# Optimization experiments

Hardware: AMD Instinct MI355X
Metric: run time of the kernel (lower is better)

## Reference

```python
import jax, jax.numpy as jnp
import numpy as np

D_MODEL = 2048
N_HEADS = 16
N_KV = 4
D_HEAD = 128
D1 = 64
D2 = 64
WSIZE = 1024
EPS = 1e-6
ROPE_BASE = 10000.0


def _rmsnorm(x):
    # RMSNorm over last dim, no affine weight
    return x * jax.lax.rsqrt(jnp.mean(x * x, axis=-1, keepdims=True) + EPS)


def _apply_rope(x, cos, sin):
    # x: (..., D2); cos/sin: (1, T, 1, D2//2)
    h = D2 // 2
    x1, x2 = x[..., :h], x[..., h:]
    return jnp.concatenate([x1 * cos + x2 * sin, -x1 * sin + x2 * cos], axis=-1)


def setup_inputs() -> dict:
    key = jax.random.key(0)
    ks = jax.random.split(key, 6)
    B, T = 2, 2048
    return {
        "hidden_states": jax.random.normal(ks[0], (B, T, D_MODEL), dtype=jnp.float32),
        "W_qkv": jax.random.normal(ks[1], (D_MODEL, (N_HEADS + N_KV) * D_HEAD), dtype=jnp.float32) * 0.02,
        "W_rk": jax.random.normal(ks[2], (D_MODEL, D2), dtype=jnp.float32) * 0.02,
        "b_rk": jax.random.normal(ks[3], (D2,), dtype=jnp.float32) * 0.02,
        "softmax_scaler": jnp.ones((N_HEADS,), dtype=jnp.float32),
        "W_g": jax.random.normal(ks[5], (D_MODEL, D_MODEL), dtype=jnp.float32) * 0.02,
    }


def reference(hidden_states, W_qkv, W_rk, b_rk, softmax_scaler, W_g):
    x = hidden_states
    B, T, _ = x.shape
    # fused qkv projection + per-(head,token) RMSNorm (qk_norm)
    qkv = (x @ W_qkv).reshape(B, T, N_HEADS + N_KV, D_HEAD)
    qkv = _rmsnorm(qkv)
    q, kv = qkv[:, :, :N_HEADS], qkv[:, :, N_HEADS:]
    q_nope, q_rope = q[..., :D1], q[..., D1:]

    # head-tied rope key: shared across all heads
    k_rope = (x @ W_rk + b_rk)[:, :, None, :]  # (B, T, 1, D2)

    # rotary embedding (start_pos = 0)
    inv_freq = 1.0 / (ROPE_BASE ** (jnp.arange(0, D2, 2, dtype=jnp.float32) / D2))
    freqs = jnp.arange(T, dtype=jnp.float32)[:, None] * inv_freq[None, :]  # (T, D2//2)
    cos = jnp.cos(freqs)[None, :, None, :]
    sin = jnp.sin(freqs)[None, :, None, :]
    q_rope = _apply_rope(q_rope, cos, sin)
    k_rope = jnp.broadcast_to(_apply_rope(k_rope, cos, sin), (B, T, N_HEADS, D2))

    q = jnp.concatenate([q_nope, q_rope], axis=-1)  # (B, T, H, D_HEAD)

    # scalable softmax: scale q by per-head scaler * log(min(pos, wsize))
    pos = jnp.arange(1, T + 1, dtype=jnp.float32)
    log_pos = jnp.log(jnp.minimum(pos, float(WSIZE)))[None, :, None, None]
    q = softmax_scaler[None, None, :, None] * log_pos * q

    # tied k/v: first D1 of kv shared between k and v; repeat kv heads (GQA)
    kv_tied, v = kv[..., :D1], kv[..., D1:]
    rep = N_HEADS // N_KV
    kv_tied = jnp.repeat(kv_tied, rep, axis=2)  # (B, T, H, D1)
    v = jnp.repeat(v, rep, axis=2)              # (B, T, H, D2)
    k = jnp.concatenate([kv_tied, k_rope], axis=-1)   # (B, T, H, D_HEAD)
    v_full = jnp.concatenate([kv_tied, v], axis=-1)   # (B, T, H, D_HEAD)

    # sliding-window causal attention: key j valid iff i - WSIZE <= j <= i
    scores = jnp.einsum('bthd,bshd->bhts', q, k) / np.float32(np.sqrt(D_HEAD))
    i = jnp.arange(T)[:, None]
    j = jnp.arange(T)[None, :]
    mask = (j <= i) & (j >= i - WSIZE)
    scores = jnp.where(mask[None, None], scores, jnp.float32(-1e30))
    p = jax.nn.softmax(scores, axis=-1)
    y = jnp.einsum('bhts,bshd->bthd', p, v_full)  # (B, T, H, D_HEAD)

    # elementwise silu gate
    g = (x @ W_g).reshape(B, T, N_HEADS, D_HEAD)
    return y * jax.nn.silu(g)
```

## Files before the change

kernel.cpp:

```cpp
#include <hip/hip_runtime.h>

typedef _Float16 f16;
typedef _Float16 half8 __attribute__((ext_vector_type(8)));
typedef _Float16 half4_t __attribute__((ext_vector_type(4)));
typedef float f32x4 __attribute__((ext_vector_type(4)));

#define T_SEQ 2048
#define B_SZ 2
#define DM 2048
#define NH 16
#define NKV 4
#define DH 128
#define NQKV 2560
#define NALL 4736
#define COL_RK 2560
#define COL_G 2688
#define M_ROWS 4096
#define WIN 1024

typedef __attribute__((address_space(1))) const unsigned int guint;
typedef __attribute__((address_space(3))) unsigned int luint;
__device__ __forceinline__ void gload16(const void* g, void* l) {
  __builtin_amdgcn_global_load_lds((guint*)g, (luint*)l, 16, 0, 0);
}

__global__ void k_cvt(const float* __restrict__ in, f16* __restrict__ out, int n) {
  int i = (blockIdx.x * 256 + threadIdx.x) * 4;
  if (i >= n) return;
  float4 v = *(const float4*)(in + i);
  half4_t o;
  o[0] = (f16)v.x; o[1] = (f16)v.y; o[2] = (f16)v.z; o[3] = (f16)v.w;
  *(half4_t*)(out + i) = o;
}

__global__ __launch_bounds__(256) void k_cvt_t(const float* __restrict__ W,
                                               f16* __restrict__ Wt, int K, int N) {
  __shared__ float tile[32][33];
  int k0 = blockIdx.x * 32, n0 = blockIdx.y * 32;
  int tx = threadIdx.x & 31, ty = threadIdx.x >> 5;
#pragma unroll
  for (int r = 0; r < 32; r += 8)
    tile[ty + r][tx] = W[(size_t)(k0 + ty + r) * N + n0 + tx];
  __syncthreads();
#pragma unroll
  for (int r = 0; r < 32; r += 8)
    Wt[(size_t)(n0 + ty + r) * K + k0 + tx] = (f16)tile[tx][ty + r];
}

__global__ __launch_bounds__(256) void k_vt(const f16* __restrict__ v, f16* __restrict__ vt) {
  __shared__ f16 tile[32][34];
  int t0 = blockIdx.x * 32, d0 = blockIdx.y * 32, m = blockIdx.z;
  int tx = threadIdx.x & 31, ty = threadIdx.x >> 5;
  const f16* src = v + (size_t)m * T_SEQ * DH;
  f16* dst = vt + (size_t)m * T_SEQ * DH;
#pragma unroll
  for (int r = 0; r < 32; r += 8)
    tile[ty + r][tx] = src[(size_t)(t0 + ty + r) * DH + d0 + tx];
  __syncthreads();
#pragma unroll
  for (int r = 0; r < 32; r += 8)
    dst[(size_t)(d0 + ty + r) * T_SEQ + t0 + tx] = tile[tx][ty + r];
}

__global__ __launch_bounds__(256) void k_gemm_lds(const f16* __restrict__ A,
                                                  const f16* __restrict__ Bt,
                                                  f16* __restrict__ C,
                                                  int N, int K) {
  __shared__ __align__(16) f16 As[128 * 32];
  __shared__ __align__(16) f16 Bs[128 * 32];
  unsigned orig = blockIdx.y * 37u + blockIdx.x;
  unsigned swz = (orig & 7u) * 148u + (orig >> 3);
  int m0 = (int)(swz / 37u) * 128;
  int n0 = (int)(swz % 37u) * 128;
  int tid = threadIdx.x, lane = tid & 63, w = tid >> 6;
  int wm = (w >> 1) * 64, wn = (w & 1) * 64;
  int fr = lane & 15, fq = lane >> 4;
  f32x4 acc[4][4] = {};
  int r0 = tid >> 2;
  int c0 = (tid & 3) * 8;
  const f16* Ag0 = A + (size_t)(m0 + r0) * K + c0;
  const f16* Ag1 = A + (size_t)(m0 + 64 + r0) * K + c0;
  const f16* Bg0 = Bt + (size_t)(n0 + r0) * K + c0;
  const f16* Bg1 = Bt + (size_t)(n0 + 64 + r0) * K + c0;
  char* Asb = (char*)As;
  char* Bsb = (char*)Bs;
  for (int k0 = 0; k0 < K; k0 += 32) {
    gload16(Ag0 + k0, Asb + w * 1024);
    gload16(Ag1 + k0, Asb + 4096 + w * 1024);
    gload16(Bg0 + k0, Bsb + w * 1024);
    gload16(Bg1 + k0, Bsb + 4096 + w * 1024);
    __syncthreads();
    half8 af[4], bf[4];
#pragma unroll
    for (int i = 0; i < 4; ++i)
      af[i] = *(const half8*)(Asb + (wm + i * 16 + fr) * 64 + fq * 16);
#pragma unroll
    for (int j = 0; j < 4; ++j)
      bf[j] = *(const half8*)(Bsb + (wn + j * 16 + fr) * 64 + fq * 16);
#pragma unroll
    for (int i = 0; i < 4; ++i)
#pragma unroll
      for (int j = 0; j < 4; ++j)
        acc[i][j] = __builtin_amdgcn_mfma_f32_16x16x32_f16(af[i], bf[j], acc[i][j], 0, 0, 0);
    __syncthreads();
  }
#pragma unroll
  for (int i = 0; i < 4; ++i) {
    int row = m0 + wm + i * 16 + fq * 4;
#pragma unroll
    for (int j = 0; j < 4; ++j) {
      int col = n0 + wn + j * 16 + fr;
      f16* Cp = C + (size_t)row * N + col;
#pragma unroll
      for (int rr = 0; rr < 4; ++rr) Cp[(size_t)rr * N] = (f16)acc[i][j][rr];
    }
  }
}

__global__ __launch_bounds__(256) void k_postproc(
    const f16* __restrict__ CA,
    const float* __restrict__ brk, const float* __restrict__ sscal,
    f16* __restrict__ q16, f16* __restrict__ k16, f16* __restrict__ v16) {
  int row = blockIdx.x;
  int b = row >> 11, t = row & 2047;
  int lane = threadIdx.x & 63, wid = threadIdx.x >> 6;
  int ridx = lane & 31;
  float inv_freq = powf(10000.0f, -(float)(2 * ridx) / 64.0f);
  float fr = (float)t * inv_freq;
  float cs = cosf(fr), sn = sinf(fr);
  float logpos = logf(fminf((float)(t + 1), 1024.0f));
  const float rsqrt_d_log2e = 0.08838834764831845f * 1.4426950408889634f;
  const f16* Crow = CA + (size_t)row * NALL;
#pragma unroll
  for (int p = 0; p < 5; ++p) {
    int h = p * 4 + wid;
    float v0 = (float)Crow[h * 128 + lane];
    float v1 = (float)Crow[h * 128 + 64 + lane];
    float ss = v0 * v0 + v1 * v1;
#pragma unroll
    for (int m = 1; m < 64; m <<= 1) ss += __shfl_xor(ss, m);
    float rms = rsqrtf(ss * (1.0f / 128.0f) + 1e-6f);
    v0 *= rms; v1 *= rms;
    if (h < NH) {
      float part = __shfl_xor(v1, 32);
      float vr = (lane < 32) ? (v1 * cs + part * sn) : (v1 * cs - part * sn);
      float scale = sscal[h] * logpos * rsqrt_d_log2e;
      size_t qb = ((size_t)(b * NH + h) * T_SEQ + t) * DH;
      q16[qb + lane]      = (f16)(v0 * scale);
      q16[qb + 64 + lane] = (f16)(vr * scale);
    } else {
      int hk = h - NH;
      size_t kb = ((size_t)(b * NKV + hk) * T_SEQ + t) * DH;
      k16[kb + lane]      = (f16)v0;
      v16[kb + lane]      = (f16)v0;
      v16[kb + 64 + lane] = (f16)v1;
    }
  }
  if (wid == 0) {
    float kr = (float)Crow[COL_RK + lane] + brk[lane];
    float part = __shfl_xor(kr, 32);
    float vr = (lane < 32) ? (kr * cs + part * sn) : (kr * cs - part * sn);
    f16 hv = (f16)vr;
#pragma unroll
    for (int hk = 0; hk < NKV; ++hk)
      k16[((size_t)(b * NKV + hk) * T_SEQ + t) * DH + 64 + lane] = hv;
  }
}

__global__ __launch_bounds__(512, 2) void k_attn(
    const f16* __restrict__ q16, const f16* __restrict__ k16, const f16* __restrict__ vt16,
    const f16* __restrict__ gA, float* __restrict__ out) {
  __shared__ __align__(16) f16 Ks[64 * DH];
  __shared__ __align__(16) f16 Vs[DH * 64];
  __shared__ __align__(16) f16 Ps[8 * 16 * 64];
  int bx = blockIdx.x;
  int qt = (bx & 1) ? (15 - (bx >> 1)) : (bx >> 1);
  int h = blockIdx.y, b = blockIdx.z, hk = h >> 2;
  int tid = threadIdx.x, lane = tid & 63, w = tid >> 6;
  int i0 = qt * 128, iw = i0 + w * 16;
  int fr = lane & 15, fq = lane >> 4;

  char* Ksb = (char*)Ks;
  char* Vsb = (char*)Vs;
  char* Psb = (char*)Ps + w * 2048;

  const f16* qbase = q16 + ((size_t)(b * NH + h) * T_SEQ + iw + fr) * DH;
  half8 qf[4];
#pragma unroll
  for (int kb = 0; kb < 4; ++kb) qf[kb] = *(const half8*)&qbase[kb * 32 + fq * 8];

  f32x4 o[8] = {};
  float mrow[4] = {-1e30f, -1e30f, -1e30f, -1e30f};
  float lrow[4] = {0.f, 0.f, 0.f, 0.f};

  const f16* kg = k16 + (size_t)(b * NKV + hk) * T_SEQ * DH;
  const f16* vg = vt16 + (size_t)(b * NKV + hk) * T_SEQ * DH;

  int jtTop = qt * 2 + 1;
  int jt0 = qt >= 8 ? qt * 2 - 16 : 0;
  for (int jt = jt0; jt <= jtTop; ++jt) {
    int j0 = jt * 64;
#pragma unroll
    for (int i = 0; i < 2; ++i) {
      int r = i * 32 + (tid >> 4);
      int c = (tid & 15) ^ (r & 7);
      gload16(kg + (size_t)(j0 + r) * DH + c * 8, Ksb + i * 8192 + w * 1024);
    }
#pragma unroll
    for (int i = 0; i < 2; ++i) {
      int r = i * 64 + (tid >> 3);
      int c = (tid & 7) ^ (r & 7);
      gload16(vg + (size_t)r * T_SEQ + j0 + c * 8, Vsb + i * 8192 + w * 1024);
    }
    __syncthreads();

    bool active = (jt == jtTop) ? (w >= 4)
                : ((qt >= 8 && jt == jt0) ? (w < 4) : true);
    if (active) {
      f32x4 s[4] = {};
      __builtin_amdgcn_s_setprio(1);
#pragma unroll
      for (int nf = 0; nf < 4; ++nf) {
        int row = nf * 16 + fr;
        int sw = fr & 7;
#pragma unroll
        for (int kb = 0; kb < 4; ++kb) {
          half8 bfv = *(const half8*)(Ksb + row * 256 + ((((kb << 2) | fq) ^ sw) << 4));
          s[nf] = __builtin_amdgcn_mfma_f32_16x16x32_f16(qf[kb], bfv, s[nf], 0, 0, 0);
        }
      }
      __builtin_amdgcn_s_setprio(0);
      int il = (w << 4) + (fq << 2);
      if (jt >= (qt << 1)) {
        int dc = (jt << 6) - i0;
#pragma unroll
        for (int nf = 0; nf < 4; ++nf) {
          int jo = nf * 16 + fr + dc;
#pragma unroll
          for (int r = 0; r < 4; ++r)
            if (jo > il + r) s[nf][r] = -3e38f;
        }
      } else if (qt >= 8 && jt - jt0 < 2) {
        int dl = (jt - jt0) << 6;
#pragma unroll
        for (int nf = 0; nf < 4; ++nf) {
          int jo = nf * 16 + fr + dl;
#pragma unroll
          for (int r = 0; r < 4; ++r)
            if (jo < il + r) s[nf][r] = -3e38f;
        }
      }
      float tm[4];
#pragma unroll
      for (int r = 0; r < 4; ++r)
        tm[r] = fmaxf(fmaxf(s[0][r], s[1][r]), fmaxf(s[2][r], s[3][r]));
#pragma unroll
      for (int r = 0; r < 4; ++r) {
        tm[r] = fmaxf(tm[r], __shfl_xor(tm[r], 1));
        tm[r] = fmaxf(tm[r], __shfl_xor(tm[r], 2));
        tm[r] = fmaxf(tm[r], __shfl_xor(tm[r], 4));
        tm[r] = fmaxf(tm[r], __shfl_xor(tm[r], 8));
      }
      bool need = false;
#pragma unroll
      for (int r = 0; r < 4; ++r) need = need || (tm[r] > mrow[r] + 8.0f);
      if (__any(need)) {
#pragma unroll
        for (int r = 0; r < 4; ++r) {
          float mn = fmaxf(mrow[r], tm[r]);
          float sc = exp2f(mrow[r] - mn);
          mrow[r] = mn;
          lrow[r] *= sc;
#pragma unroll
          for (int of = 0; of < 8; ++of) o[of][r] *= sc;
        }
      }
      float ls[4] = {0.f, 0.f, 0.f, 0.f};
#pragma unroll
      for (int nf = 0; nf < 4; ++nf)
#pragma unroll
        for (int r = 0; r < 4; ++r) {
          float pv = exp2f(s[nf][r] - mrow[r]);
          s[nf][r] = pv;
          ls[r] += pv;
        }
#pragma unroll
      for (int r = 0; r < 4; ++r) {
        float t2 = ls[r];
        t2 += __shfl_xor(t2, 1); t2 += __shfl_xor(t2, 2);
        t2 += __shfl_xor(t2, 4); t2 += __shfl_xor(t2, 8);
        lrow[r] += t2;
      }
#pragma unroll
      for (int nf = 0; nf < 4; ++nf) {
        int sbase = (nf << 1) + (fr >> 3);
        int boff = (fr & 7) << 1;
#pragma unroll
        for (int r = 0; r < 4; ++r) {
          int q = (fq << 2) + r;
          *(f16*)(Psb + q * 128 + ((sbase ^ (q & 7)) << 4) + boff) = (f16)s[nf][r];
        }
      }
      asm volatile("s_waitcnt lgkmcnt(0)" ::: "memory");
      __builtin_amdgcn_sched_barrier(0);
      half8 pf0 = *(const half8*)(Psb + fr * 128 + (((fq) ^ (fr & 7)) << 4));
      half8 pf1 = *(const half8*)(Psb + fr * 128 + (((4 | fq) ^ (fr & 7)) << 4));
      __builtin_amdgcn_s_setprio(1);
#pragma unroll
      for (int of = 0; of < 8; ++of) {
        int vrow0 = of * 16 + fr;
        int sw = fr & 7;
        half8 v0 = *(const half8*)(Vsb + vrow0 * 128 + ((fq ^ sw) << 4));
        half8 v1 = *(const half8*)(Vsb + vrow0 * 128 + (((4 | fq) ^ sw) << 4));
        o[of] = __builtin_amdgcn_mfma_f32_16x16x32_f16(pf0, v0, o[of], 0, 0, 0);
        o[of] = __builtin_amdgcn_mfma_f32_16x16x32_f16(pf1, v1, o[of], 0, 0, 0);
      }
      __builtin_amdgcn_s_setprio(0);
    }
    __syncthreads();
  }
  const f16* gb = gA + ((size_t)(b * T_SEQ) + iw) * NALL + COL_G + h * DH;
  float* ob = out + ((size_t)(b * T_SEQ) + iw) * DM + h * DH;
#pragma unroll
  for (int r = 0; r < 4; ++r) {
    float inv = 1.0f / lrow[r];
    int ir = fq * 4 + r;
#pragma unroll
    for (int of = 0; of < 8; ++of) {
      int d = of * 16 + fr;
      float gv = (float)gb[(size_t)ir * NALL + d];
      float sig = gv / (1.0f + expf(-gv));
      ob[(size_t)ir * DM + d] = o[of][r] * inv * sig;
    }
  }
}

extern "C" void kernel_launch(void* const* d_in, const int* in_sizes, int n_in,
                              void* d_out, int out_size, void* d_ws, size_t ws_size,
                              hipStream_t stream) {
  const float* x     = (const float*)d_in[0];
  const float* Wqkv  = (const float*)d_in[1];
  const float* Wrk   = (const float*)d_in[2];
  const float* brk   = (const float*)d_in[3];
  const float* sscal = (const float*)d_in[4];
  const float* Wg    = (const float*)d_in[5];
  float* out = (float*)d_out;
  char* ws = (char*)d_ws;
  size_t off = 0;
  auto alloc = [&](size_t bytes) -> void* {
    void* p = ws + off;
    off += (bytes + 255) & ~(size_t)255;
    return p;
  };
  f16* x16     = (f16*)alloc((size_t)M_ROWS * DM * 2);
  f16* BtAll   = (f16*)alloc((size_t)NALL * DM * 2);
  f16* CAll    = (f16*)alloc((size_t)M_ROWS * NALL * 2);
  f16* q16     = (f16*)alloc((size_t)B_SZ * NH * T_SEQ * DH * 2);
  f16* k16     = (f16*)alloc((size_t)B_SZ * NKV * T_SEQ * DH * 2);
  f16* v16     = (f16*)alloc((size_t)B_SZ * NKV * T_SEQ * DH * 2);
  f16* vt16    = (f16*)alloc((size_t)B_SZ * NKV * T_SEQ * DH * 2);

  k_cvt<<<(M_ROWS * DM / 4 + 255) / 256, 256, 0, stream>>>(x, x16, M_ROWS * DM);
  k_cvt_t<<<dim3(DM / 32, NQKV / 32), 256, 0, stream>>>(Wqkv, BtAll, DM, NQKV);
  k_cvt_t<<<dim3(DM / 32, 64 / 32), 256, 0, stream>>>(Wrk, BtAll + (size_t)COL_RK * DM, DM, 64);
  k_cvt_t<<<dim3(DM / 32, DM / 32), 256, 0, stream>>>(Wg, BtAll + (size_t)COL_G * DM, DM, DM);

  k_gemm_lds<<<dim3(NALL / 128, M_ROWS / 128), 256, 0, stream>>>(x16, BtAll, CAll, NALL, DM);

  k_postproc<<<M_ROWS, 256, 0, stream>>>(CAll, brk, sscal, q16, k16, v16);
  k_vt<<<dim3(T_SEQ / 32, DH / 32, B_SZ * NKV), 256, 0, stream>>>(v16, vt16);

  k_attn<<<dim3(T_SEQ / 128, NH, B_SZ), 512, 0, stream>>>(q16, k16, vt16, CAll, out);
}
```

Measured before the change: 367.2 us.

## Rewrite fused projection GEMM with double-buffered LDS, 256x128 tiles, swizzle

Replaces the single-buffered 128x128 GEMM with a 512-thread 256x128-tile kernel that loads K=64 slabs into double-buffered LDS, so the global loads for the next slab overlap MFMA work. It adds an XOR swizzle on LDS columns to cut bank conflicts and raises wave priority during MFMAs. The output row stride is padded to 4864 so the tile grid divides evenly, and the downstream kernels read with the padded stride. The padded B rows are never initialized, so those columns compute garbage that nothing reads. The 96KB LDS footprint also limits how many blocks fit per CU.

Result: faster. 360.0 us (-2.0%).

```diff
diff --git a/kernel.cpp b/kernel.cpp
--- a/kernel.cpp
+++ b/kernel.cpp
@@ -13,6 +13,7 @@
 #define DH 128
 #define NQKV 2560
 #define NALL 4736
+#define NALLP 4864
 #define COL_RK 2560
 #define COL_G 2688
 #define M_ROWS 4096
@@ -62,57 +63,84 @@
     dst[(size_t)(d0 + ty + r) * T_SEQ + t0 + tx] = tile[tx][ty + r];
 }
 
-__global__ __launch_bounds__(256) void k_gemm_lds(const f16* __restrict__ A,
+#define GEMM_PHASE(cb, kk, sb, koff)                                                        \
+  {                                                                                         \
+    char* Ab = lds + (cb) * 32768 + (kk) * 16384;                                           \
+    char* Bb = lds + 65536 + (cb) * 16384 + (kk) * 8192;                                    \
+    half8 af[4], bf[4];                                                                     \
+    _Pragma("unroll")                                                                       \
+    for (int i = 0; i < 4; ++i)                                                             \
+      af[i] = *(const half8*)(Ab + (wm * 64 + i * 16 + fr) * 64 + xsl);                     \
+    _Pragma("unroll")                                                                       \
+    for (int j = 0; j < 4; ++j)                                                             \
+      bf[j] = *(const half8*)(Bb + (wn * 64 + j * 16 + fr) * 64 + xsl);                     \
+    gload16(Ag0 + (koff) + (kk) * 32, lds + (sb) * 32768 + (kk) * 16384 + w * 1024);        \
+    gload16(Ag1 + (koff) + (kk) * 32, lds + (sb) * 32768 + (kk) * 16384 + 8192 + w * 1024); \
+    gload16(Bg + (koff) + (kk) * 32, lds + 65536 + (sb) * 16384 + (kk) * 8192 + w * 1024);  \
+    __builtin_amdgcn_s_barrier();                                                           \
+    __builtin_amdgcn_sched_barrier(0);                                                      \
+    asm volatile("s_waitcnt lgkmcnt(0)" ::: "memory");                                      \
+    __builtin_amdgcn_sched_barrier(0);                                                      \
+    __builtin_amdgcn_s_setprio(1);                                                          \
+    _Pragma("unroll")                                                                       \
+    for (int i = 0; i < 4; ++i)                                                             \
+      _Pragma("unroll")                                                                     \
+      for (int j = 0; j < 4; ++j)                                                           \
+        acc[i][j] = __builtin_amdgcn_mfma_f32_16x16x32_f16(af[i], bf[j], acc[i][j], 0, 0, 0); \
+    __builtin_amdgcn_s_setprio(0);                                                          \
+    asm volatile("s_waitcnt vmcnt(3)" ::: "memory");                                        \
+    __builtin_amdgcn_s_barrier();                                                           \
+    __builtin_amdgcn_sched_barrier(0);                                                      \
+  }
+
+__global__ __launch_bounds__(512, 2) void k_gemm8(const f16* __restrict__ A,
                                                   const f16* __restrict__ Bt,
-                                                  f16* __restrict__ C,
-                                                  int N, int K) {
-  __shared__ __align__(16) f16 As[128 * 32];
-  __shared__ __align__(16) f16 Bs[128 * 32];
-  unsigned orig = blockIdx.y * 37u + blockIdx.x;
-  unsigned swz = (orig & 7u) * 148u + (orig >> 3);
-  int m0 = (int)(swz / 37u) * 128;
-  int n0 = (int)(swz % 37u) * 128;
+                                                  f16* __restrict__ C) {
+  __shared__ __align__(16) char lds[98304];
+  const int K = DM;
+  unsigned orig = blockIdx.y * 38u + blockIdx.x;
+  unsigned swz = (orig & 7u) * 76u + (orig >> 3);
+  int m0 = (int)(swz / 38u) * 256;
+  int n0 = (int)(swz % 38u) * 128;
   int tid = threadIdx.x, lane = tid & 63, w = tid >> 6;
-  int wm = (w >> 1) * 64, wn = (w & 1) * 64;
+  int wm = w >> 1, wn = w & 1;
   int fr = lane & 15, fq = lane >> 4;
+  int xsl = (fq ^ ((fr >> 1) & 3)) << 4;
+  int sr = tid >> 2, ss = tid & 3;
+  int scol = (ss ^ ((sr >> 1) & 3)) * 8;
   f32x4 acc[4][4] = {};
-  int r0 = tid >> 2;
-  int c0 = (tid & 3) * 8;
-  const f16* Ag0 = A + (size_t)(m0 + r0) * K + c0;
-  const f16* Ag1 = A + (size_t)(m0 + 64 + r0) * K + c0;
-  const f16* Bg0 = Bt + (size_t)(n0 + r0) * K + c0;
-  const f16* Bg1 = Bt + (size_t)(n0 + 64 + r0) * K + c0;
-  char* Asb = (char*)As;
-  char* Bsb = (char*)Bs;
-  for (int k0 = 0; k0 < K; k0 += 32) {
-    gload16(Ag0 + k0, Asb + w * 1024);
-    gload16(Ag1 + k0, Asb + 4096 + w * 1024);
-    gload16(Bg0 + k0, Bsb + w * 1024);
-    gload16(Bg1 + k0, Bsb + 4096 + w * 1024);
-    __syncthreads();
-    half8 af[4], bf[4];
-#pragma unroll
-    for (int i = 0; i < 4; ++i)
-      af[i] = *(const half8*)(Asb + (wm + i * 16 + fr) * 64 + fq * 16);
-#pragma unroll
-    for (int j = 0; j < 4; ++j)
-      bf[j] = *(const half8*)(Bsb + (wn + j * 16 + fr) * 64 + fq * 16);
-#pragma unroll
-    for (int i = 0; i < 4; ++i)
-#pragma unroll
-      for (int j = 0; j < 4; ++j)
-        acc[i][j] = __builtin_amdgcn_mfma_f32_16x16x32_f16(af[i], bf[j], acc[i][j], 0, 0, 0);
-    __syncthreads();
-  }
+  const f16* Ag0 = A + (size_t)(m0 + sr) * K + scol;
+  const f16* Ag1 = A + (size_t)(m0 + 128 + sr) * K + scol;
+  const f16* Bg  = Bt + (size_t)(n0 + sr) * K + scol;
+
+  gload16(Ag0, lds + w * 1024);
+  gload16(Ag1, lds + 8192 + w * 1024);
+  gload16(Bg, lds + 65536 + w * 1024);
+  gload16(Ag0 + 32, lds + 16384 + w * 1024);
+  gload16(Ag1 + 32, lds + 16384 + 8192 + w * 1024);
+  gload16(Bg + 32, lds + 65536 + 8192 + w * 1024);
+  asm volatile("s_waitcnt vmcnt(3)" ::: "memory");
+  __builtin_amdgcn_s_barrier();
+  __builtin_amdgcn_sched_barrier(0);
+
+  for (int kt = 0; kt < 32; ++kt) {
+    int cb = kt & 1;
+    int nt = kt < 31 ? kt + 1 : 31;
+    int sb = nt & 1;
+    int koff = nt * 64;
+    GEMM_PHASE(cb, 0, sb, koff);
+    GEMM_PHASE(cb, 1, sb, koff);
+  }
+
 #pragma unroll
   for (int i = 0; i < 4; ++i) {
-    int row = m0 + wm + i * 16 + fq * 4;
+    int row = m0 + wm * 64 + i * 16 + fq * 4;
 #pragma unroll
     for (int j = 0; j < 4; ++j) {
-      int col = n0 + wn + j * 16 + fr;
-      f16* Cp = C + (size_t)row * N + col;
-#pragma unroll
-      for (int rr = 0; rr < 4; ++rr) Cp[(size_t)rr * N] = (f16)acc[i][j][rr];
+      int col = n0 + wn * 64 + j * 16 + fr;
+      f16* Cp = C + (size_t)row * NALLP + col;
+#pragma unroll
+      for (int rr = 0; rr < 4; ++rr) Cp[(size_t)rr * NALLP] = (f16)acc[i][j][rr];
     }
   }
 }
@@ -130,7 +158,7 @@
   float cs = cosf(fr), sn = sinf(fr);
   float logpos = logf(fminf((float)(t + 1), 1024.0f));
   const float rsqrt_d_log2e = 0.08838834764831845f * 1.4426950408889634f;
-  const f16* Crow = CA + (size_t)row * NALL;
+  const f16* Crow = CA + (size_t)row * NALLP;
 #pragma unroll
   for (int p = 0; p < 5; ++p) {
     int h = p * 4 + wid;
@@ -319,7 +347,7 @@
     }
     __syncthreads();
   }
-  const f16* gb = gA + ((size_t)(b * T_SEQ) + iw) * NALL + COL_G + h * DH;
+  const f16* gb = gA + ((size_t)(b * T_SEQ) + iw) * NALLP + COL_G + h * DH;
   float* ob = out + ((size_t)(b * T_SEQ) + iw) * DM + h * DH;
 #pragma unroll
   for (int r = 0; r < 4; ++r) {
@@ -328,7 +356,7 @@
 #pragma unroll
     for (int of = 0; of < 8; ++of) {
       int d = of * 16 + fr;
-      float gv = (float)gb[(size_t)ir * NALL + d];
+      float gv = (float)gb[(size_t)ir * NALLP + d];
       float sig = gv / (1.0f + expf(-gv));
       ob[(size_t)ir * DM + d] = o[of][r] * inv * sig;
     }
@@ -353,8 +381,8 @@
     return p;
   };
   f16* x16     = (f16*)alloc((size_t)M_ROWS * DM * 2);
-  f16* BtAll   = (f16*)alloc((size_t)NALL * DM * 2);
-  f16* CAll    = (f16*)alloc((size_t)M_ROWS * NALL * 2);
+  f16* BtAll   = (f16*)alloc((size_t)NALLP * DM * 2);
+  f16* CAll    = (f16*)alloc((size_t)M_ROWS * NALLP * 2);
   f16* q16     = (f16*)alloc((size_t)B_SZ * NH * T_SEQ * DH * 2);
   f16* k16     = (f16*)alloc((size_t)B_SZ * NKV * T_SEQ * DH * 2);
   f16* v16     = (f16*)alloc((size_t)B_SZ * NKV * T_SEQ * DH * 2);
@@ -365,7 +393,7 @@
   k_cvt_t<<<dim3(DM / 32, 64 / 32), 256, 0, stream>>>(Wrk, BtAll + (size_t)COL_RK * DM, DM, 64);
   k_cvt_t<<<dim3(DM / 32, DM / 32), 256, 0, stream>>>(Wg, BtAll + (size_t)COL_G * DM, DM, DM);
 
-  k_gemm_lds<<<dim3(NALL / 128, M_ROWS / 128), 256, 0, stream>>>(x16, BtAll, CAll, NALL, DM);
+  k_gemm8<<<dim3(NALLP / 128, M_ROWS / 256), 512, 0, stream>>>(x16, BtAll, CAll);
 
   k_postproc<<<M_ROWS, 256, 0, stream>>>(CAll, brk, sscal, q16, k16, v16);
   k_vt<<<dim3(T_SEQ / 32, DH / 32, B_SZ * NKV), 256, 0, stream>>>(v16, vt16);
```
